# Performance work log

Hardware: AMD Instinct MI355X
Metric: run time of the kernel (lower is better)

Reference implementation:

```python
import jax, jax.numpy as jnp
import numpy as np

TOP_K = 30
NUM_RBF = 16
MAX_REL = 32          # max_relative_feature
EDGE_FEATURES = 128
NUM_POS_EMB = 16
EDGE_INS = NUM_POS_EMB + NUM_RBF * 25  # 416
ONEHOT_DIM = 2 * MAX_REL + 2           # 66

# 25 (A, B) atom-pair indices into stacked order [Ca, N, C, O, Cb]
PAIR_A = np.array([0,1,2,3,4, 0,0,0,0, 1,1,1, 4,4, 3, 1,2,3,4, 2,3,4, 2,3, 2])
PAIR_B = np.array([0,1,2,3,4, 1,2,3,4, 2,3,4, 2,3, 2, 0,0,0,0, 1,1,1, 4,4, 3])


def setup_inputs() -> dict:
    key = jax.random.key(0)
    k1, k2, k3, k4, k5 = jax.random.split(key, 5)
    B, L = 4, 2048
    X = jax.random.normal(k1, (B, L, 4, 3), dtype=jnp.float32)
    mask = jnp.ones((B, L), dtype=jnp.float32)
    residue_idx = jnp.arange(B * L, dtype=jnp.int64 if jax.config.jax_enable_x64 else jnp.int32).reshape(B, L)
    # parameters
    W_pos = jax.random.normal(k2, (ONEHOT_DIM, NUM_POS_EMB), dtype=jnp.float32) * 0.02
    b_pos = jnp.zeros((NUM_POS_EMB,), dtype=jnp.float32)
    W_edge = jax.random.normal(k3, (EDGE_INS, EDGE_FEATURES), dtype=jnp.float32) * 0.02
    ln_gamma = jnp.ones((EDGE_FEATURES,), dtype=jnp.float32)
    ln_beta = jnp.zeros((EDGE_FEATURES,), dtype=jnp.float32)
    return {"X": X, "mask": mask, "residue_idx": residue_idx,
            "W_pos": W_pos, "b_pos": b_pos, "W_edge": W_edge,
            "ln_gamma": ln_gamma, "ln_beta": ln_beta}


def reference(X, mask, residue_idx, W_pos, b_pos, W_edge, ln_gamma, ln_beta):
    eps = 1e-6
    Bsz, L = X.shape[0], X.shape[1]
    K = min(TOP_K, L)

    # virtual Cb construction
    b = X[:, :, 1, :] - X[:, :, 0, :]
    c = X[:, :, 2, :] - X[:, :, 1, :]
    a = jnp.cross(b, c)
    Cb = -0.58273431 * a + 0.56802827 * b - 0.54067466 * c + X[:, :, 1, :]
    Ca = X[:, :, 1, :]
    N_ = X[:, :, 0, :]
    C_ = X[:, :, 2, :]
    O_ = X[:, :, 3, :]

    # --- _dist on Ca: masked pairwise distance + top-k smallest ---
    mask2d = mask[:, None, :] * mask[:, :, None]              # [B, L, L]
    dX = Ca[:, :, None, :] - Ca[:, None, :, :]                # [B, L, L, 3]
    D = mask2d * jnp.sqrt(jnp.sum(dX * dX, axis=-1) + eps)    # [B, L, L]
    D_max = jnp.max(D, axis=-1, keepdims=True)
    D_adjust = D + (1.0 - mask2d) * D_max
    neg_vals, E_idx = jax.lax.top_k(-D_adjust, K)             # smallest-k, ascending

    # --- 25 atom-pair distances, gathered only at neighbor indices ---
    atoms = jnp.stack([Ca, N_, C_, O_, Cb], axis=0)           # [5, B, L, 3]
    A_all = atoms[PAIR_A]                                     # [25, B, L, 3]
    B_all = atoms[PAIR_B]                                     # [25, B, L, 3]
    # gather neighbor coords: [25, B, L, K, 3]
    gather_b = jax.vmap(lambda coords, idx: coords[idx], in_axes=(0, 0))      # over batch
    gather_pb = jax.vmap(gather_b, in_axes=(0, None))                         # over pairs
    B_nb = gather_pb(B_all, E_idx)
    diff = A_all[:, :, :, None, :] - B_nb
    D_nb = jnp.sqrt(jnp.sum(diff * diff, axis=-1) + 1e-6)     # [25, B, L, K]

    # --- RBF featurization ---
    D_mu = jnp.linspace(2.0, 22.0, NUM_RBF, dtype=D_nb.dtype)
    D_sigma = (22.0 - 2.0) / NUM_RBF
    RBF = jnp.exp(-(((D_nb[..., None] - D_mu) / D_sigma) ** 2))  # [25, B, L, K, R]
    # concat order: [B, L, K, 25*R]
    RBF_all = jnp.transpose(RBF, (1, 2, 3, 0, 4)).reshape(Bsz, L, K, 25 * NUM_RBF)

    # --- relative positional encodings ---
    offset = residue_idx[:, :, None] - residue_idx[:, None, :]    # [B, L, L]
    off_nb = jnp.take_along_axis(offset, E_idx, axis=2)           # [B, L, K]
    d = jnp.clip(off_nb + MAX_REL, 0, 2 * MAX_REL)
    d_onehot = jax.nn.one_hot(d, ONEHOT_DIM, dtype=W_pos.dtype)   # [B, L, K, 66]
    E_pos = d_onehot @ W_pos + b_pos                              # [B, L, K, 16]

    # --- edge embedding + layernorm ---
    E = jnp.concatenate([E_pos, RBF_all], axis=-1)                # [B, L, K, 416]
    E = E @ W_edge                                                # [B, L, K, 128]
    mu = jnp.mean(E, axis=-1, keepdims=True)
    var = jnp.mean((E - mu) ** 2, axis=-1, keepdims=True)
    E = (E - mu) / jnp.sqrt(var + 1e-5) * ln_gamma + ln_beta
    return E
```

## Files before the change

kernel.cpp:

```cpp
#include <hip/hip_runtime.h>
#include <hip/hip_bf16.h>
#include <math.h>

#define BB      4
#define LL      2048
#define KNB     30
#define NRES    (BB*LL)
#define NEDGE   (NRES*KNB)
#define EDGE_IN 416
#define KT      13
#define ME      32
#define AST3    168
#define FINF    3.4e38f
#define LOG2E   1.44269504088896340736f

typedef __attribute__((ext_vector_type(8))) _Float16 half8;
typedef __attribute__((ext_vector_type(4))) float floatx4;

__device__ __constant__ int d_PA[25] = {0,1,2,3,4,0,0,0,0,1,1,1,4,4,3,1,2,3,4,2,3,4,2,3,2};
__device__ __constant__ int d_PB[25] = {0,1,2,3,4,1,2,3,4,2,3,4,2,3,2,0,0,0,0,1,1,1,4,4,3};

__device__ __forceinline__ unsigned short f2h_bits(float x) {
    _Float16 h = (_Float16)x;
    union { _Float16 h; unsigned short u; } v; v.h = h;
    return v.u;
}
__device__ __forceinline__ unsigned pack2h(float a, float b) {
    return (unsigned)f2h_bits(a) | ((unsigned)f2h_bits(b) << 16);
}

__global__ __launch_bounds__(256) void atoms_kernel(const float* __restrict__ X,
                                                    float* __restrict__ atoms,
                                                    float* __restrict__ caTx,
                                                    float* __restrict__ caTy,
                                                    float* __restrict__ caTz) {
    int r = blockIdx.x * blockDim.x + threadIdx.x;
    if (r >= NRES) return;
    const float* xr = X + (size_t)r * 12;
    float Nx = xr[0],  Ny = xr[1],  Nz = xr[2];
    float Ax = xr[3],  Ay = xr[4],  Az = xr[5];
    float Cx = xr[6],  Cy = xr[7],  Cz = xr[8];
    float Ox = xr[9],  Oy = xr[10], Oz = xr[11];
    float bx = Ax - Nx, by = Ay - Ny, bz = Az - Nz;
    float cx = Cx - Ax, cy = Cy - Ay, cz = Cz - Az;
    float ax = by * cz - bz * cy;
    float ay = bz * cx - bx * cz;
    float az = bx * cy - by * cx;
    float Cbx = -0.58273431f * ax + 0.56802827f * bx - 0.54067466f * cx + Ax;
    float Cby = -0.58273431f * ay + 0.56802827f * by - 0.54067466f * cy + Ay;
    float Cbz = -0.58273431f * az + 0.56802827f * bz - 0.54067466f * cz + Az;
    float* o = atoms + (size_t)r * 15;
    o[0]  = Ax;  o[1]  = Ay;  o[2]  = Az;
    o[3]  = Nx;  o[4]  = Ny;  o[5]  = Nz;
    o[6]  = Cx;  o[7]  = Cy;  o[8]  = Cz;
    o[9]  = Ox;  o[10] = Oy;  o[11] = Oz;
    o[12] = Cbx; o[13] = Cby; o[14] = Cbz;
    caTx[r] = Ax; caTy[r] = Ay; caTz[r] = Az;
}

__global__ __launch_bounds__(256, 6) void topk_kernel(const float* __restrict__ caTx,
                                                      const float* __restrict__ caTy,
                                                      const float* __restrict__ caTz,
                                                      const float* __restrict__ mask,
                                                      int* __restrict__ E_idx) {
#pragma clang fp contract(off)
    int t    = threadIdx.x;
    int wid  = t >> 6;
    int lane = t & 63;
    int bi   = blockIdx.x * 4 + wid;
    int b    = bi >> 11;
    int j0   = b << 11;

    float cx = caTx[bi], cy = caTy[bi], cz = caTz[bi];
    float mi = mask[bi];

    float aa[32];
    float lmax = 0.0f;
#pragma unroll
    for (int i = 0; i < 32; i++) {
        int j = j0 + i * 64 + lane;
        float dx = cx - caTx[j], dy = cy - caTy[j], dz = cz - caTz[j];
        float ssq = ((dx * dx + dy * dy) + dz * dz) + 1e-6f;
        float m2  = mask[j] * mi;
        float Dj  = m2 * sqrtf(ssq);
        aa[i] = Dj;
        lmax = fmaxf(lmax, Dj);
    }
    for (int off = 32; off; off >>= 1) lmax = fmaxf(lmax, __shfl_xor(lmax, off));

    float l0 = FINF, l1 = FINF, l2 = FINF, l3 = FINF;
    int   i0 = 0,    i1 = 0,    i2 = 0,    i3 = 0;
#pragma unroll
    for (int i = 0; i < 32; i++) {
        float m2 = mask[j0 + i * 64 + lane] * mi;
        float v  = aa[i] + (1.0f - m2) * lmax;
        aa[i] = v;
        bool c0 = v < l0, c1 = v < l1, c2 = v < l2, c3 = v < l3;
        l3 = c2 ? l2 : (c3 ? v : l3);  i3 = c2 ? i2 : (c3 ? i : i3);
        l2 = c1 ? l1 : (c2 ? v : l2);  i2 = c1 ? i1 : (c2 ? i : i2);
        l1 = c0 ? l0 : (c1 ? v : l1);  i1 = c0 ? i0 : (c1 ? i : i1);
        l0 = c0 ? v  : l0;             i0 = c0 ? i  : i0;
    }

    unsigned consumed = 0;
    int* outp = E_idx + (size_t)bi * KNB;
#pragma unroll 1
    for (int r = 0; r < KNB; r++) {
        float bv = l0;
        int   bj = (i0 << 6) | lane;
        for (int off = 1; off < 64; off <<= 1) {
            float ov = __shfl_xor(bv, off);
            int   oj = __shfl_xor(bj, off);
            if (ov < bv || (ov == bv && oj < bj)) { bv = ov; bj = oj; }
        }
        if (lane == 0) outp[r] = bj;
        bool mine = ((bj & 63) == lane);
        if (mine) {
            consumed |= 1u << ((unsigned)bj >> 6);
            l0 = l1; i0 = i1;
            l1 = l2; i1 = i2;
            l2 = l3; i2 = i3;
            l3 = FINF;
        }
        bool need = mine && (l0 == FINF) && (r < KNB - 1);
        if (need) {
            l0 = FINF; l1 = FINF; l2 = FINF; l3 = FINF;
            i0 = 0; i1 = 0; i2 = 0; i3 = 0;
#pragma unroll
            for (int i = 0; i < 32; i++) {
                float v = (consumed & (1u << i)) ? FINF : aa[i];
                bool c0 = v < l0, c1 = v < l1, c2 = v < l2, c3 = v < l3;
                l3 = c2 ? l2 : (c3 ? v : l3);  i3 = c2 ? i2 : (c3 ? i : i3);
                l2 = c1 ? l1 : (c2 ? v : l2);  i2 = c1 ? i1 : (c2 ? i : i2);
                l1 = c0 ? l0 : (c1 ? v : l1);  i1 = c0 ? i0 : (c1 ? i : i1);
                l0 = c0 ? v  : l0;             i0 = c0 ? i  : i0;
            }
        }
    }
}

__global__ __launch_bounds__(256) void wprep_kernel(const float* __restrict__ W_edge,
                                                    half8* __restrict__ Wfh,
                                                    half8* __restrict__ Wfl) {
    int t = blockIdx.x * blockDim.x + threadIdx.x;
    if (t >= KT * 8 * 64) return;
    int kk   = t >> 9;
    int rem  = t & 511;
    int nt   = rem >> 6;
    int lane = rem & 63;
    int n  = nt * 16 + (lane & 15);
    int kb = kk * 32 + (lane >> 4) * 8;
    half8 vh, vl;
#pragma unroll
    for (int j = 0; j < 8; j++) {
        float w = W_edge[(size_t)(kb + j) * 128 + n];
        _Float16 wh = (_Float16)w;
        vh[j] = wh;
        vl[j] = (_Float16)(w - (float)wh);
    }
    Wfh[t] = vh;
    Wfl[t] = vl;
}

__global__ __launch_bounds__(256) void edge_kernel(const float* __restrict__ atoms,
                                                   const int* __restrict__ E_idx,
                                                   const int* __restrict__ resi,
                                                   const float* __restrict__ W_pos,
                                                   const float* __restrict__ b_pos,
                                                   const half8* __restrict__ Wfh,
                                                   const half8* __restrict__ Wfl,
                                                   const float* __restrict__ gamma,
                                                   const float* __restrict__ beta,
                                                   float* __restrict__ out) {
    __shared__ _Float16 Ah[ME * AST3];
    __shared__ _Float16 Al[ME * AST3];
    __shared__ float Dl[ME][26];
    __shared__ float redS[2][ME];
    __shared__ int   s_gi[ME], s_gj[ME], s_d[ME];

    int t  = threadIdx.x;
    int e0 = blockIdx.x * ME;

    if (t < ME) {
        int e  = e0 + t;
        int gi = e / KNB;
        int k  = e - gi * KNB;
        int b  = gi >> 11;
        int j  = E_idx[(size_t)gi * KNB + k];
        s_gi[t] = gi;
        s_gj[t] = (b << 11) + j;
        int off = resi[gi] - resi[(b << 11) + j];
        int d = off + 32;
        s_d[t] = d < 0 ? 0 : (d > 64 ? 64 : d);
    }
    __syncthreads();

    for (int idx = t; idx < ME * 25; idx += 256) {
        int e = idx / 25, p = idx - e * 25;
        const float* Ar = atoms + (size_t)s_gi[e] * 15 + d_PA[p] * 3;
        const float* Br = atoms + (size_t)s_gj[e] * 15 + d_PB[p] * 3;
        float dx = Ar[0] - Br[0];
        float dy = Ar[1] - Br[1];
        float dz = Ar[2] - Br[2];
        Dl[e][p] = sqrtf(dx * dx + dy * dy + dz * dz + 1e-6f);
    }
    __syncthreads();

    int fe  = t >> 3;
    int fj8 = t & 7;
    const float* dle = Dl[fe];
    _Float16* fah = &Ah[fe * AST3];
    _Float16* fal = &Al[fe * AST3];

    {
        if (fj8 < 4) {
            int c = fj8 * 4;
            int dpos = s_d[fe];
            const float* wp = W_pos + dpos * 16 + c;
            float v[4];
#pragma unroll
            for (int q = 0; q < 4; q++) v[q] = wp[q] + b_pos[c + q];
            float h0 = (float)(_Float16)v[0], h1 = (float)(_Float16)v[1];
            float h2 = (float)(_Float16)v[2], h3 = (float)(_Float16)v[3];
            *(unsigned*)&fah[c + 0] = pack2h(v[0], v[1]);
            *(unsigned*)&fah[c + 2] = pack2h(v[2], v[3]);
            *(unsigned*)&fal[c + 0] = pack2h(v[0] - h0, v[1] - h1);
            *(unsigned*)&fal[c + 2] = pack2h(v[2] - h2, v[3] - h3);
        }
#pragma unroll
        for (int i = 0; i < 9; i++) {
            int c2 = 2 * (fj8 + 8 * i);
            int p  = c2 >> 4;
            int r  = c2 & 15;
            float D = dle[p];
            float mu0 = 2.0f + (float)r * (20.0f / 15.0f);
            float mu1 = 2.0f + (float)(r + 1) * (20.0f / 15.0f);
            float t0 = (D - mu0) * 0.8f;
            float t1 = (D - mu1) * 0.8f;
            float g0 = __builtin_amdgcn_exp2f(-(t0 * t0) * LOG2E);
            float g1 = __builtin_amdgcn_exp2f(-(t1 * t1) * LOG2E);
            float h0 = (float)(_Float16)g0, h1 = (float)(_Float16)g1;
            *(unsigned*)&fah[16 + c2] = pack2h(g0, g1);
            *(unsigned*)&fal[16 + c2] = pack2h(g0 - h0, g1 - h1);
        }
    }
    __syncthreads();

    int lane  = t & 63;
    int w     = t >> 6;
    int strip = (w & 1) * 16;
    int h     = w >> 1;
    int m     = lane & 15;
    int quad  = lane >> 4;
    const _Float16* pah = &Ah[(strip + m) * AST3 + quad * 8];
    const _Float16* pal = &Al[(strip + m) * AST3 + quad * 8];

    floatx4 acc[4];
#pragma unroll
    for (int c = 0; c < 4; c++) acc[c] = (floatx4){0.f, 0.f, 0.f, 0.f};

    half8 bh[4], bl[4], bnh[4], bnl[4];
#pragma unroll
    for (int c = 0; c < 4; c++) {
        int idx = (h * 4 + c) * 64 + lane;
        bh[c] = Wfh[idx];
        bl[c] = Wfl[idx];
    }

#pragma unroll 1
    for (int kk = 0; kk < 5; kk++) {
        half8 a_hi = *(const half8*)(pah + kk * 32);
        half8 a_lo = *(const half8*)(pal + kk * 32);
#pragma unroll
        for (int c = 0; c < 4; c++) {
            int idx = ((kk + 1) * 8 + h * 4 + c) * 64 + lane;
            bnh[c] = Wfh[idx];
            bnl[c] = Wfl[idx];
        }
#pragma unroll
        for (int c = 0; c < 4; c++) {
            acc[c] = __builtin_amdgcn_mfma_f32_16x16x32_f16(a_hi, bh[c], acc[c], 0, 0, 0);
            acc[c] = __builtin_amdgcn_mfma_f32_16x16x32_f16(a_lo, bh[c], acc[c], 0, 0, 0);
            acc[c] = __builtin_amdgcn_mfma_f32_16x16x32_f16(a_hi, bl[c], acc[c], 0, 0, 0);
        }
#pragma unroll
        for (int c = 0; c < 4; c++) { bh[c] = bnh[c]; bl[c] = bnl[c]; }
    }

    __syncthreads();

    {
#pragma unroll
        for (int i = 9; i < 17; i++) {
            int c2 = 2 * (fj8 + 8 * i);
            int p  = c2 >> 4;
            int r  = c2 & 15;
            float D = dle[p];
            float mu0 = 2.0f + (float)r * (20.0f / 15.0f);
            float mu1 = 2.0f + (float)(r + 1) * (20.0f / 15.0f);
            float t0 = (D - mu0) * 0.8f;
            float t1 = (D - mu1) * 0.8f;
            float g0 = __builtin_amdgcn_exp2f(-(t0 * t0) * LOG2E);
            float g1 = __builtin_amdgcn_exp2f(-(t1 * t1) * LOG2E);
            float h0 = (float)(_Float16)g0, h1 = (float)(_Float16)g1;
            int col = c2 - 144;
            *(unsigned*)&fah[col] = pack2h(g0, g1);
            *(unsigned*)&fal[col] = pack2h(g0 - h0, g1 - h1);
        }
    }
    __syncthreads();

#pragma unroll 1
    for (int kk = 5; kk < 9; kk++) {
        half8 a_hi = *(const half8*)(pah + (kk - 5) * 32);
        half8 a_lo = *(const half8*)(pal + (kk - 5) * 32);
#pragma unroll
        for (int c = 0; c < 4; c++) {
            int idx = ((kk + 1) * 8 + h * 4 + c) * 64 + lane;
            bnh[c] = Wfh[idx];
            bnl[c] = Wfl[idx];
        }
#pragma unroll
        for (int c = 0; c < 4; c++) {
            acc[c] = __builtin_amdgcn_mfma_f32_16x16x32_f16(a_hi, bh[c], acc[c], 0, 0, 0);
            acc[c] = __builtin_amdgcn_mfma_f32_16x16x32_f16(a_lo, bh[c], acc[c], 0, 0, 0);
            acc[c] = __builtin_amdgcn_mfma_f32_16x16x32_f16(a_hi, bl[c], acc[c], 0, 0, 0);
        }
#pragma unroll
        for (int c = 0; c < 4; c++) { bh[c] = bnh[c]; bl[c] = bnl[c]; }
    }

    __syncthreads();

    {
#pragma unroll
        for (int i = 17; i < 25; i++) {
            int c2 = 2 * (fj8 + 8 * i);
            int p  = c2 >> 4;
            int r  = c2 & 15;
            float D = dle[p];
            float mu0 = 2.0f + (float)r * (20.0f / 15.0f);
            float mu1 = 2.0f + (float)(r + 1) * (20.0f / 15.0f);
            float t0 = (D - mu0) * 0.8f;
            float t1 = (D - mu1) * 0.8f;
            float g0 = __builtin_amdgcn_exp2f(-(t0 * t0) * LOG2E);
            float g1 = __builtin_amdgcn_exp2f(-(t1 * t1) * LOG2E);
            float h0 = (float)(_Float16)g0, h1 = (float)(_Float16)g1;
            int col = c2 - 272;
            *(unsigned*)&fah[col] = pack2h(g0, g1);
            *(unsigned*)&fal[col] = pack2h(g0 - h0, g1 - h1);
        }
    }
    __syncthreads();

#pragma unroll 1
    for (int kk = 9; kk < KT; kk++) {
        half8 a_hi = *(const half8*)(pah + (kk - 9) * 32);
        half8 a_lo = *(const half8*)(pal + (kk - 9) * 32);
        if (kk < KT - 1) {
#pragma unroll
            for (int c = 0; c < 4; c++) {
                int idx = ((kk + 1) * 8 + h * 4 + c) * 64 + lane;
                bnh[c] = Wfh[idx];
                bnl[c] = Wfl[idx];
            }
        }
#pragma unroll
        for (int c = 0; c < 4; c++) {
            acc[c] = __builtin_amdgcn_mfma_f32_16x16x32_f16(a_hi, bh[c], acc[c], 0, 0, 0);
            acc[c] = __builtin_amdgcn_mfma_f32_16x16x32_f16(a_lo, bh[c], acc[c], 0, 0, 0);
            acc[c] = __builtin_amdgcn_mfma_f32_16x16x32_f16(a_hi, bl[c], acc[c], 0, 0, 0);
        }
#pragma unroll
        for (int c = 0; c < 4; c++) { bh[c] = bnh[c]; bl[c] = bnl[c]; }
    }

    int elb = strip + quad * 4;
    float sarr[4];
#pragma unroll
    for (int r = 0; r < 4; r++) {
        float s = acc[0][r] + acc[1][r] + acc[2][r] + acc[3][r];
        for (int msk = 1; msk <= 8; msk <<= 1) s += __shfl_xor(s, msk);
        sarr[r] = s;
    }
    if (m == 0) {
#pragma unroll
        for (int r = 0; r < 4; r++) redS[h][elb + r] = sarr[r];
    }
    __syncthreads();
    float mu[4];
#pragma unroll
    for (int r = 0; r < 4; r++) mu[r] = (redS[0][elb + r] + redS[1][elb + r]) * (1.0f / 128.0f);
    __syncthreads();
    float dvv[4][4];
#pragma unroll
    for (int r = 0; r < 4; r++) {
        float v = 0.f;
#pragma unroll
        for (int c = 0; c < 4; c++) { dvv[c][r] = acc[c][r] - mu[r]; v += dvv[c][r] * dvv[c][r]; }
        for (int msk = 1; msk <= 8; msk <<= 1) v += __shfl_xor(v, msk);
        if (m == 0) redS[h][elb + r] = v;
    }
    __syncthreads();
#pragma unroll
    for (int r = 0; r < 4; r++) {
        float var  = (redS[0][elb + r] + redS[1][elb + r]) * (1.0f / 128.0f);
        float rstd = rsqrtf(var + 1e-5f);
        int e = e0 + elb + r;
        float* orow = out + (size_t)e * 128;
#pragma unroll
        for (int c = 0; c < 4; c++) {
            int n = (h * 4 + c) * 16 + m;
            orow[n] = dvv[c][r] * rstd * gamma[n] + beta[n];
        }
    }
}

extern "C" void kernel_launch(void* const* d_in, const int* in_sizes, int n_in,
                              void* d_out, int out_size, void* d_ws, size_t ws_size,
                              hipStream_t stream) {
    const float* X      = (const float*)d_in[0];
    const float* mask   = (const float*)d_in[1];
    const int*   resi   = (const int*)  d_in[2];
    const float* W_pos  = (const float*)d_in[3];
    const float* b_pos  = (const float*)d_in[4];
    const float* W_edge = (const float*)d_in[5];
    const float* gamma  = (const float*)d_in[6];
    const float* beta   = (const float*)d_in[7];
    float* out = (float*)d_out;

    float* atoms = (float*)d_ws;
    int*   E_idx = (int*)((char*)d_ws + (size_t)NRES * 15 * 4);
    half8* Wfh   = (half8*)((char*)d_ws + 1474560);
    half8* Wfl   = (half8*)((char*)d_ws + 1581056);
    float* caTx  = (float*)((char*)d_ws + 1687552);
    float* caTy  = (float*)((char*)d_ws + 1720320);
    float* caTz  = (float*)((char*)d_ws + 1753088);

    atoms_kernel<<<(NRES + 255) / 256, 256, 0, stream>>>(X, atoms, caTx, caTy, caTz);
    wprep_kernel<<<(KT * 8 * 64 + 255) / 256, 256, 0, stream>>>(W_edge, Wfh, Wfl);
    topk_kernel<<<NRES / 4, 256, 0, stream>>>(caTx, caTy, caTz, mask, E_idx);
    edge_kernel<<<NEDGE / ME, 256, 0, stream>>>(atoms, E_idx, resi,
                                                W_pos, b_pos, Wfh, Wfl, gamma, beta, out);
}
```

Before: 320.7 us.

## Double edges per block so each wave reuses weight fragments across two M strips

Raises the edge tile per block from 32 to 64 and has each wave compute two 16-row strips against the same B fragments. The goal is to halve global weight loads per edge and interleave independent MFMA chains. Featurization remaps threads to four per edge, and the LayerNorm epilogue loops over both strips. The cost is doubled LDS tiles and accumulators, which may reduce occupancy, and half as many blocks.

New measurement: 291.8 us. -9.0%, faster.

```diff
diff --git a/kernel.cpp b/kernel.cpp
--- a/kernel.cpp
+++ b/kernel.cpp
@@ -9,7 +9,7 @@
 #define NEDGE   (NRES*KNB)
 #define EDGE_IN 416
 #define KT      13
-#define ME      32
+#define ME      64
 #define AST3    168
 #define FINF    3.4e38f
 #define LOG2E   1.44269504088896340736f
@@ -206,15 +206,15 @@
     }
     __syncthreads();
 
-    int fe  = t >> 3;
-    int fj8 = t & 7;
+    int fe  = t >> 2;
+    int fj4 = t & 3;
     const float* dle = Dl[fe];
     _Float16* fah = &Ah[fe * AST3];
     _Float16* fal = &Al[fe * AST3];
 
     {
-        if (fj8 < 4) {
-            int c = fj8 * 4;
+        {
+            int c = fj4 * 4;
             int dpos = s_d[fe];
             const float* wp = W_pos + dpos * 16 + c;
             float v[4];
@@ -228,8 +228,8 @@
             *(unsigned*)&fal[c + 2] = pack2h(v[2] - h2, v[3] - h3);
         }
 #pragma unroll
-        for (int i = 0; i < 9; i++) {
-            int c2 = 2 * (fj8 + 8 * i);
+        for (int i = 0; i < 18; i++) {
+            int c2 = 2 * (fj4 + 4 * i);
             int p  = c2 >> 4;
             int r  = c2 & 15;
             float D = dle[p];
@@ -248,16 +248,18 @@
 
     int lane  = t & 63;
     int w     = t >> 6;
-    int strip = (w & 1) * 16;
+    int ms    = w & 1;
     int h     = w >> 1;
     int m     = lane & 15;
     int quad  = lane >> 4;
-    const _Float16* pah = &Ah[(strip + m) * AST3 + quad * 8];
-    const _Float16* pal = &Al[(strip + m) * AST3 + quad * 8];
-
-    floatx4 acc[4];
-#pragma unroll
-    for (int c = 0; c < 4; c++) acc[c] = (floatx4){0.f, 0.f, 0.f, 0.f};
+    const _Float16* pah = &Ah[(ms * 32 + m) * AST3 + quad * 8];
+    const _Float16* pal = &Al[(ms * 32 + m) * AST3 + quad * 8];
+
+    floatx4 acc[2][4];
+#pragma unroll
+    for (int s = 0; s < 2; s++)
+#pragma unroll
+        for (int c = 0; c < 4; c++) acc[s][c] = (floatx4){0.f, 0.f, 0.f, 0.f};
 
     half8 bh[4], bl[4], bnh[4], bnl[4];
 #pragma unroll
@@ -269,8 +271,10 @@
 
 #pragma unroll 1
     for (int kk = 0; kk < 5; kk++) {
-        half8 a_hi = *(const half8*)(pah + kk * 32);
-        half8 a_lo = *(const half8*)(pal + kk * 32);
+        half8 a_hi0 = *(const half8*)(pah + kk * 32);
+        half8 a_lo0 = *(const half8*)(pal + kk * 32);
+        half8 a_hi1 = *(const half8*)(pah + 16 * AST3 + kk * 32);
+        half8 a_lo1 = *(const half8*)(pal + 16 * AST3 + kk * 32);
 #pragma unroll
         for (int c = 0; c < 4; c++) {
             int idx = ((kk + 1) * 8 + h * 4 + c) * 64 + lane;
@@ -279,9 +283,12 @@
         }
 #pragma unroll
         for (int c = 0; c < 4; c++) {
-            acc[c] = __builtin_amdgcn_mfma_f32_16x16x32_f16(a_hi, bh[c], acc[c], 0, 0, 0);
-            acc[c] = __builtin_amdgcn_mfma_f32_16x16x32_f16(a_lo, bh[c], acc[c], 0, 0, 0);
-            acc[c] = __builtin_amdgcn_mfma_f32_16x16x32_f16(a_hi, bl[c], acc[c], 0, 0, 0);
+            acc[0][c] = __builtin_amdgcn_mfma_f32_16x16x32_f16(a_hi0, bh[c], acc[0][c], 0, 0, 0);
+            acc[1][c] = __builtin_amdgcn_mfma_f32_16x16x32_f16(a_hi1, bh[c], acc[1][c], 0, 0, 0);
+            acc[0][c] = __builtin_amdgcn_mfma_f32_16x16x32_f16(a_lo0, bh[c], acc[0][c], 0, 0, 0);
+            acc[1][c] = __builtin_amdgcn_mfma_f32_16x16x32_f16(a_lo1, bh[c], acc[1][c], 0, 0, 0);
+            acc[0][c] = __builtin_amdgcn_mfma_f32_16x16x32_f16(a_hi0, bl[c], acc[0][c], 0, 0, 0);
+            acc[1][c] = __builtin_amdgcn_mfma_f32_16x16x32_f16(a_hi1, bl[c], acc[1][c], 0, 0, 0);
         }
 #pragma unroll
         for (int c = 0; c < 4; c++) { bh[c] = bnh[c]; bl[c] = bnl[c]; }
@@ -291,8 +298,8 @@
 
     {
 #pragma unroll
-        for (int i = 9; i < 17; i++) {
-            int c2 = 2 * (fj8 + 8 * i);
+        for (int i = 18; i < 34; i++) {
+            int c2 = 2 * (fj4 + 4 * i);
             int p  = c2 >> 4;
             int r  = c2 & 15;
             float D = dle[p];
@@ -312,8 +319,10 @@
 
 #pragma unroll 1
     for (int kk = 5; kk < 9; kk++) {
-        half8 a_hi = *(const half8*)(pah + (kk - 5) * 32);
-        half8 a_lo = *(const half8*)(pal + (kk - 5) * 32);
+        half8 a_hi0 = *(const half8*)(pah + (kk - 5) * 32);
+        half8 a_lo0 = *(const half8*)(pal + (kk - 5) * 32);
+        half8 a_hi1 = *(const half8*)(pah + 16 * AST3 + (kk - 5) * 32);
+        half8 a_lo1 = *(const half8*)(pal + 16 * AST3 + (kk - 5) * 32);
 #pragma unroll
         for (int c = 0; c < 4; c++) {
             int idx = ((kk + 1) * 8 + h * 4 + c) * 64 + lane;
@@ -322,9 +331,12 @@
         }
 #pragma unroll
         for (int c = 0; c < 4; c++) {
-            acc[c] = __builtin_amdgcn_mfma_f32_16x16x32_f16(a_hi, bh[c], acc[c], 0, 0, 0);
-            acc[c] = __builtin_amdgcn_mfma_f32_16x16x32_f16(a_lo, bh[c], acc[c], 0, 0, 0);
-            acc[c] = __builtin_amdgcn_mfma_f32_16x16x32_f16(a_hi, bl[c], acc[c], 0, 0, 0);
+            acc[0][c] = __builtin_amdgcn_mfma_f32_16x16x32_f16(a_hi0, bh[c], acc[0][c], 0, 0, 0);
+            acc[1][c] = __builtin_amdgcn_mfma_f32_16x16x32_f16(a_hi1, bh[c], acc[1][c], 0, 0, 0);
+            acc[0][c] = __builtin_amdgcn_mfma_f32_16x16x32_f16(a_lo0, bh[c], acc[0][c], 0, 0, 0);
+            acc[1][c] = __builtin_amdgcn_mfma_f32_16x16x32_f16(a_lo1, bh[c], acc[1][c], 0, 0, 0);
+            acc[0][c] = __builtin_amdgcn_mfma_f32_16x16x32_f16(a_hi0, bl[c], acc[0][c], 0, 0, 0);
+            acc[1][c] = __builtin_amdgcn_mfma_f32_16x16x32_f16(a_hi1, bl[c], acc[1][c], 0, 0, 0);
         }
 #pragma unroll
         for (int c = 0; c < 4; c++) { bh[c] = bnh[c]; bl[c] = bnl[c]; }
@@ -334,8 +346,8 @@
 
     {
 #pragma unroll
-        for (int i = 17; i < 25; i++) {
-            int c2 = 2 * (fj8 + 8 * i);
+        for (int i = 34; i < 50; i++) {
+            int c2 = 2 * (fj4 + 4 * i);
             int p  = c2 >> 4;
             int r  = c2 & 15;
             float D = dle[p];
@@ -355,8 +367,10 @@
 
 #pragma unroll 1
     for (int kk = 9; kk < KT; kk++) {
-        half8 a_hi = *(const half8*)(pah + (kk - 9) * 32);
-        half8 a_lo = *(const half8*)(pal + (kk - 9) * 32);
+        half8 a_hi0 = *(const half8*)(pah + (kk - 9) * 32);
+        half8 a_lo0 = *(const half8*)(pal + (kk - 9) * 32);
+        half8 a_hi1 = *(const half8*)(pah + 16 * AST3 + (kk - 9) * 32);
+        half8 a_lo1 = *(const half8*)(pal + 16 * AST3 + (kk - 9) * 32);
         if (kk < KT - 1) {
 #pragma unroll
             for (int c = 0; c < 4; c++) {
@@ -367,52 +381,59 @@
         }
 #pragma unroll
         for (int c = 0; c < 4; c++) {
-            acc[c] = __builtin_amdgcn_mfma_f32_16x16x32_f16(a_hi, bh[c], acc[c], 0, 0, 0);
-            acc[c] = __builtin_amdgcn_mfma_f32_16x16x32_f16(a_lo, bh[c], acc[c], 0, 0, 0);
-            acc[c] = __builtin_amdgcn_mfma_f32_16x16x32_f16(a_hi, bl[c], acc[c], 0, 0, 0);
+            acc[0][c] = __builtin_amdgcn_mfma_f32_16x16x32_f16(a_hi0, bh[c], acc[0][c], 0, 0, 0);
+            acc[1][c] = __builtin_amdgcn_mfma_f32_16x16x32_f16(a_hi1, bh[c], acc[1][c], 0, 0, 0);
+            acc[0][c] = __builtin_amdgcn_mfma_f32_16x16x32_f16(a_lo0, bh[c], acc[0][c], 0, 0, 0);
+            acc[1][c] = __builtin_amdgcn_mfma_f32_16x16x32_f16(a_lo1, bh[c], acc[1][c], 0, 0, 0);
+            acc[0][c] = __builtin_amdgcn_mfma_f32_16x16x32_f16(a_hi0, bl[c], acc[0][c], 0, 0, 0);
+            acc[1][c] = __builtin_amdgcn_mfma_f32_16x16x32_f16(a_hi1, bl[c], acc[1][c], 0, 0, 0);
         }
 #pragma unroll
         for (int c = 0; c < 4; c++) { bh[c] = bnh[c]; bl[c] = bnl[c]; }
     }
 
-    int elb = strip + quad * 4;
-    float sarr[4];
-#pragma unroll
-    for (int r = 0; r < 4; r++) {
-        float s = acc[0][r] + acc[1][r] + acc[2][r] + acc[3][r];
-        for (int msk = 1; msk <= 8; msk <<= 1) s += __shfl_xor(s, msk);
-        sarr[r] = s;
-    }
-    if (m == 0) {
-#pragma unroll
-        for (int r = 0; r < 4; r++) redS[h][elb + r] = sarr[r];
-    }
-    __syncthreads();
-    float mu[4];
-#pragma unroll
-    for (int r = 0; r < 4; r++) mu[r] = (redS[0][elb + r] + redS[1][elb + r]) * (1.0f / 128.0f);
-    __syncthreads();
-    float dvv[4][4];
-#pragma unroll
-    for (int r = 0; r < 4; r++) {
-        float v = 0.f;
-#pragma unroll
-        for (int c = 0; c < 4; c++) { dvv[c][r] = acc[c][r] - mu[r]; v += dvv[c][r] * dvv[c][r]; }
-        for (int msk = 1; msk <= 8; msk <<= 1) v += __shfl_xor(v, msk);
-        if (m == 0) redS[h][elb + r] = v;
-    }
-    __syncthreads();
-#pragma unroll
-    for (int r = 0; r < 4; r++) {
-        float var  = (redS[0][elb + r] + redS[1][elb + r]) * (1.0f / 128.0f);
-        float rstd = rsqrtf(var + 1e-5f);
-        int e = e0 + elb + r;
-        float* orow = out + (size_t)e * 128;
-#pragma unroll
-        for (int c = 0; c < 4; c++) {
-            int n = (h * 4 + c) * 16 + m;
-            orow[n] = dvv[c][r] * rstd * gamma[n] + beta[n];
-        }
+#pragma unroll
+    for (int s = 0; s < 2; s++) {
+        int elb = ms * 32 + s * 16 + quad * 4;
+        float sarr[4];
+#pragma unroll
+        for (int r = 0; r < 4; r++) {
+            float sm = acc[s][0][r] + acc[s][1][r] + acc[s][2][r] + acc[s][3][r];
+            for (int msk = 1; msk <= 8; msk <<= 1) sm += __shfl_xor(sm, msk);
+            sarr[r] = sm;
+        }
+        if (m == 0) {
+#pragma unroll
+            for (int r = 0; r < 4; r++) redS[h][elb + r] = sarr[r];
+        }
+        __syncthreads();
+        float mu[4];
+#pragma unroll
+        for (int r = 0; r < 4; r++) mu[r] = (redS[0][elb + r] + redS[1][elb + r]) * (1.0f / 128.0f);
+        __syncthreads();
+        float dvv[4][4];
+#pragma unroll
+        for (int r = 0; r < 4; r++) {
+            float v = 0.f;
+#pragma unroll
+            for (int c = 0; c < 4; c++) { dvv[c][r] = acc[s][c][r] - mu[r]; v += dvv[c][r] * dvv[c][r]; }
+            for (int msk = 1; msk <= 8; msk <<= 1) v += __shfl_xor(v, msk);
+            if (m == 0) redS[h][elb + r] = v;
+        }
+        __syncthreads();
+#pragma unroll
+        for (int r = 0; r < 4; r++) {
+            float var  = (redS[0][elb + r] + redS[1][elb + r]) * (1.0f / 128.0f);
+            float rstd = rsqrtf(var + 1e-5f);
+            int e = e0 + elb + r;
+            float* orow = out + (size_t)e * 128;
+#pragma unroll
+            for (int c = 0; c < 4; c++) {
+                int n = (h * 4 + c) * 16 + m;
+                orow[n] = dvv[c][r] * rstd * gamma[n] + beta[n];
+            }
+        }
+        if (s == 0) __syncthreads();
     }
 }
 
```
